# Kernel tuning notes

Measured on AMD Instinct MI355X. Metric: run time of the kernel, lower is better.

The kernel has to match this reference:

```python
import jax, jax.numpy as jnp
import numpy as np

N, B, E, H, G, L = 128, 2, 512, 1024, 50, 3
RBF_RADIUS = 12.0
AVG_LEN = 60.0


def _resmlp(h, Win, bin_, Wh, bh, Wout, bout):
    # input proj + activation, residual hidden blocks, linear head
    h = jax.nn.gelu(h @ Win + bin_, approximate=False)
    for i in range(Wh.shape[0]):  # fixed small number of layers
        h = h + jax.nn.gelu(h @ Wh[i] + bh[i], approximate=False)
    return h @ Wout + bout


def setup_inputs() -> dict:
    key = jax.random.key(0)
    ks = jax.random.split(key, 20)
    s_in = 1.0 / np.sqrt(3 * E)
    s_h = 1.0 / np.sqrt(H)
    s_g = 1.0 / np.sqrt(G)
    return {
        'x': jax.random.normal(ks[0], (N, B, E), jnp.float32),
        'dist': jax.random.uniform(ks[1], (N, N, B), jnp.float32),
        'vec_hat': jax.random.normal(ks[2], (N, N, B, 3), jnp.float32),
        'mask': jnp.ones((B, N), dtype=bool),
        'rbf_W': jax.random.normal(ks[3], (G, E), jnp.float32) * s_g,
        'rbf_b': jnp.zeros((E,), jnp.float32),
        'e_Win': jax.random.normal(ks[4], (3 * E, H), jnp.float32) * s_in,
        'e_bin': jnp.zeros((H,), jnp.float32),
        'e_Wh': jax.random.normal(ks[5], (L, H, H), jnp.float32) * s_h,
        'e_bh': jnp.zeros((L, H), jnp.float32),
        'e_Wout': jax.random.normal(ks[6], (H, 1), jnp.float32) * s_h,
        'e_bout': jnp.zeros((1,), jnp.float32),
        'f_Win': jax.random.normal(ks[7], (3 * E, H), jnp.float32) * s_in,
        'f_bin': jnp.zeros((H,), jnp.float32),
        'f_Wh': jax.random.normal(ks[8], (L, H, H), jnp.float32) * s_h,
        'f_bh': jnp.zeros((L, H), jnp.float32),
        'f_Wout': jax.random.normal(ks[9], (H, 1), jnp.float32) * s_h,
        'f_bout': jnp.zeros((1,), jnp.float32),
    }


def reference(x, dist, vec_hat, mask, rbf_W, rbf_b, e_Win, e_bin, e_Wh, e_bh,
              e_Wout, e_bout, f_Win, f_bin, f_Wh, f_bh, f_Wout, f_bout):
    # Gaussian RBF expansion + linear projection to embed_dim
    offset = jnp.linspace(0.0, RBF_RADIUS, G)
    coeff = -0.5 / (offset[1] - offset[0]) ** 2
    g = jnp.exp(coeff * (dist[..., None] - offset) ** 2)       # (N,N,B,G)
    rbf = g @ rbf_W + rbf_b                                    # (N,N,B,E)

    # all-pairs concat feature: [x_i, x_j, rbf_ij]  -> (N,N,B,3E)
    feat = jnp.concatenate([
        jnp.broadcast_to(x[:, None], rbf.shape),
        jnp.broadcast_to(x[None, :], rbf.shape),
        rbf,
    ], axis=-1)

    entries = (mask.T[:, None] & mask.T[None, :])[..., None].astype(feat.dtype)  # (N,N,B,1)

    energy_pairs = _resmlp(feat, e_Win, e_bin, e_Wh, e_bh, e_Wout, e_bout)       # (N,N,B,1)
    force_pairs = _resmlp(feat, f_Win, f_bin, f_Wh, f_bh, f_Wout, f_bout) * vec_hat  # (N,N,B,3)

    energy = (energy_pairs * entries).sum((0, 1)) / AVG_LEN ** 2  # (B,1)
    forces = (force_pairs * entries).sum(0) / AVG_LEN             # (N,B,3)
    # torch: forces.transpose(0,1)[mask]; mask is all-True here, so this is a reshape
    forces = jnp.swapaxes(forces, 0, 1).reshape(-1, 3)            # (B*N,3)
    return energy, forces
```

## Files before the change

### kernel.cpp

```cpp
#include <hip/hip_runtime.h>
#include <stdint.h>

typedef __bf16 bf16x8 __attribute__((ext_vector_type(8)));
typedef __bf16 bf16x4 __attribute__((ext_vector_type(4)));
typedef float  f32x4  __attribute__((ext_vector_type(4)));
typedef unsigned int u32;

__device__ __forceinline__ void gl_lds16(const void* gptr, void* lptr) {
    __builtin_amdgcn_global_load_lds(
        (const __attribute__((address_space(1))) u32*)gptr,
        (__attribute__((address_space(3))) u32*)lptr,
        16, 0, 0);
}

__device__ __forceinline__ float gelu_f(float x) {
    float u = 0.7978845608f * x * (1.0f + 0.044715f * x * x);
    float e = __expf(2.0f * u);
    float t = 1.0f - 2.0f / (e + 1.0f);
    return 0.5f * x * (1.0f + t);
}

#define MEMFENCE __asm__ __volatile__("" ::: "memory")

__global__ void zero_out(float* __restrict__ o, int n) {
    int i = blockIdx.x * 256 + threadIdx.x;
    if (i < n) o[i] = 0.0f;
}

__global__ __launch_bounds__(256)
void transpose_multi(const float* __restrict__ src0, const float* __restrict__ src1,
                     __bf16* __restrict__ dst0, __bf16* __restrict__ dst1,
                     int K, int Ncols, int perBranch) {
    const int z = blockIdx.z;
    const int branch = z / perBranch;
    const int l = z - branch * perBranch;
    const size_t elems = (size_t)K * Ncols;
    const float* src = (branch ? src1 : src0) + (size_t)l * elems;
    __bf16* dst = (branch ? dst1 : dst0) + (size_t)l * elems;

    __shared__ float tile[64][65];
    const int bk = blockIdx.x * 64;
    const int bn = blockIdx.y * 64;
    const int tid = threadIdx.x;
    const int tr = tid >> 4;
    const int tc = (tid & 15) * 4;
#pragma unroll
    for (int p = 0; p < 4; ++p) {
        const int r = tr + p * 16;
        float4 v = *(const float4*)&src[(size_t)(bk + r) * Ncols + bn + tc];
        tile[r][tc] = v.x; tile[r][tc + 1] = v.y;
        tile[r][tc + 2] = v.z; tile[r][tc + 3] = v.w;
    }
    __syncthreads();
#pragma unroll
    for (int p = 0; p < 4; ++p) {
        const int rn = tr + p * 16;
        bf16x4 o;
        o[0] = (__bf16)tile[tc + 0][rn];
        o[1] = (__bf16)tile[tc + 1][rn];
        o[2] = (__bf16)tile[tc + 2][rn];
        o[3] = (__bf16)tile[tc + 3][rn];
        *(bf16x4*)&dst[(size_t)(bn + rn) * K + bk + tc] = o;
    }
}

__global__ void f32_to_bf16(const float* __restrict__ s, __bf16* __restrict__ d, int n) {
    int idx = blockIdx.x * 256 + threadIdx.x;
    if (idx * 4 < n) {
        float4 v = *(const float4*)(s + idx * 4);
        bf16x4 o;
        o[0] = (__bf16)v.x; o[1] = (__bf16)v.y; o[2] = (__bf16)v.z; o[3] = (__bf16)v.w;
        *(bf16x4*)(d + idx * 4) = o;
    }
}

__global__ void build_M1(const float* __restrict__ rbfW, const float* __restrict__ rbf_b,
                         __bf16* __restrict__ M1) {
    int t = blockIdx.x * 256 + threadIdx.x;
    int r = t >> 8;
    int c = (t & 255) * 2;
    float v0 = 0.f, v1 = 0.f;
    if (r < 50)       { v0 = rbfW[r * 512 + c]; v1 = rbfW[r * 512 + c + 1]; }
    else if (r == 50) { v0 = rbf_b[c];          v1 = rbf_b[c + 1]; }
    M1[r * 512 + c] = (__bf16)v0;
    M1[r * 512 + c + 1] = (__bf16)v1;
}

__global__ __launch_bounds__(256)
void build_G(const float* __restrict__ dist, __bf16* __restrict__ G) {
    const int t = threadIdx.x;
    const int row = blockIdx.x * 32 + (t >> 3);
    const int c0 = (t & 7) * 8;
    const float sp = 12.0f / 49.0f;
    const float coeff = -0.5f / (sp * sp);
    const float d = dist[row];
    bf16x8 v;
#pragma unroll
    for (int q = 0; q < 8; ++q) {
        const int k = c0 + q;
        float val;
        if (k < 50)       { float tt = d - (float)k * sp; val = __expf(coeff * tt * tt); }
        else if (k == 50) val = 1.0f;
        else              val = 0.0f;
        v[q] = (__bf16)val;
    }
    *(bf16x8*)(G + (size_t)row * 64 + c0) = v;
}

template <int NK, int NBN, int MODE, bool DUAL, int MINW, bool SWZ>
__global__ __launch_bounds__(256, MINW)
void gemm_k(const __bf16* __restrict__ A0, const __bf16* __restrict__ A1,
            const __bf16* __restrict__ B0, const __bf16* __restrict__ B1,
            int lda, int ldb, int ldc,
            const float* __restrict__ bias0, const float* __restrict__ bias1,
            __bf16* __restrict__ C0, __bf16* __restrict__ C1,
            float* __restrict__ Cf0, float* __restrict__ Cf1,
            const float* __restrict__ P0, const float* __restrict__ P1,
            const float* __restrict__ wout0, const float* __restrict__ wout1,
            float* __restrict__ dot0, float* __restrict__ dot1) {
    constexpr int NBS = (NBN == 16) ? 4 : (NBN == 8) ? 3 : 0;
    __shared__ __align__(16) __bf16 As[3][128 * 32];
    __shared__ __align__(16) __bf16 Bs[3][128 * 32];

    const int tid = threadIdx.x;
    int bn, bm, branch = 0;
    if constexpr (SWZ) {
        const int x = blockIdx.x & 7;
        const int slot = blockIdx.x >> 3;
        bn = slot & (NBN - 1);
        int grp = x + ((slot >> NBS) << 3);
        if constexpr (DUAL) {
            const int half = (gridDim.x >> NBS) >> 1;
            branch = (grp >= half);
            if (branch) grp -= half;
        }
        bm = grp;
    } else {
        int f2 = blockIdx.x;
        if constexpr (DUAL) {
            const int half = gridDim.x >> 1;
            branch = (f2 >= half);
            if (branch) f2 -= half;
        }
        bn = f2 & (NBN - 1);
        bm = f2 >> NBS;
    }
    const int w = tid >> 6;
    const int lane = tid & 63;

    const __bf16* Ab = (DUAL && branch) ? A1 : A0;
    const __bf16* Bb = (DUAL && branch) ? B1 : B0;

    const int r0 = tid >> 2;
    const int s0 = tid & 3;
    const char* gA0 = (const char*)Ab + (size_t)(bm * 128 + r0) * lda + s0 * 16;
    const char* gA1 = gA0 + (size_t)64 * lda;
    const char* gB0 = (const char*)Bb + (size_t)(bn * 128 + r0) * ldb + s0 * 16;
    const char* gB1 = gB0 + (size_t)64 * ldb;

    char* lA0 = (char*)&As[0][0] + w * 1024;
    char* lA1 = (char*)&As[1][0] + w * 1024;
    char* lA2 = (char*)&As[2][0] + w * 1024;
    char* lB0 = (char*)&Bs[0][0] + w * 1024;
    char* lB1 = (char*)&Bs[1][0] + w * 1024;
    char* lB2 = (char*)&Bs[2][0] + w * 1024;

    const int wm = (w >> 1) & 1;
    const int wn = w & 1;
    const int lm = lane & 15;
    const int ko = (lane >> 4) << 3;
    const int fo = (wm * 64 + lm) * 32 + ko;
    const int go = (wn * 64 + lm) * 32 + ko;
    const __bf16* pA0 = &As[0][0] + fo;
    const __bf16* pA1 = &As[1][0] + fo;
    const __bf16* pA2 = &As[2][0] + fo;
    const __bf16* pB0 = &Bs[0][0] + go;
    const __bf16* pB1 = &Bs[1][0] + go;
    const __bf16* pB2 = &Bs[2][0] + go;

    f32x4 acc[4][4];
    const f32x4 zero = {0.0f, 0.0f, 0.0f, 0.0f};
#pragma unroll
    for (int i = 0; i < 4; ++i)
#pragma unroll
        for (int j = 0; j < 4; ++j) acc[i][j] = zero;

    auto stage = [&](int buf) {
        char* la = (buf == 0) ? lA0 : (buf == 1) ? lA1 : lA2;
        char* lb = (buf == 0) ? lB0 : (buf == 1) ? lB1 : lB2;
        gl_lds16(gA0, la); gl_lds16(gA1, la + 4096);
        gl_lds16(gB0, lb); gl_lds16(gB1, lb + 4096);
        gA0 += 64; gA1 += 64; gB0 += 64; gB1 += 64;
    };
    auto compute = [&](int buf) {
        const __bf16* pa = (buf == 0) ? pA0 : (buf == 1) ? pA1 : pA2;
        const __bf16* pb = (buf == 0) ? pB0 : (buf == 1) ? pB1 : pB2;
        bf16x8 af[4], bfg[4];
#pragma unroll
        for (int i = 0; i < 4; ++i) {
            af[i]  = *(const bf16x8*)(pa + i * 512);
            bfg[i] = *(const bf16x8*)(pb + i * 512);
        }
#pragma unroll
        for (int mi = 0; mi < 4; ++mi)
#pragma unroll
            for (int ni = 0; ni < 4; ++ni)
                acc[mi][ni] = __builtin_amdgcn_mfma_f32_16x16x32_bf16(
                    af[mi], bfg[ni], acc[mi][ni], 0, 0, 0);
    };
    auto iterstep = [&](int cbuf, int sbuf) {
        MEMFENCE;
        __builtin_amdgcn_s_waitcnt(0xF74);
        __builtin_amdgcn_s_barrier();
        MEMFENCE;
        compute(cbuf);
        MEMFENCE;
        stage(sbuf);
        MEMFENCE;
    };

    stage(0);
    stage(1);
    constexpr int NIT = NK - 2;
    constexpr int NG = NIT / 3;
    constexpr int NR = NIT % 3;
    for (int g = 0; g < NG; ++g) {
        iterstep(0, 2);
        iterstep(1, 0);
        iterstep(2, 1);
    }
    if constexpr (NR >= 1) iterstep(0, 2);
    if constexpr (NR >= 2) iterstep(1, 0);
    MEMFENCE;
    __builtin_amdgcn_s_waitcnt(0xF74);
    __builtin_amdgcn_s_barrier();
    MEMFENCE;
    compute((NK - 2) % 3);
    MEMFENCE;
    __builtin_amdgcn_s_waitcnt(0xF70);
    __builtin_amdgcn_s_barrier();
    MEMFENCE;
    compute((NK - 1) % 3);

    const int col0 = bn * 128 + wn * 64 + lm;
    const int row0 = bm * 128 + wm * 64 + ((lane >> 4) << 2);
    const int ldaE = lda >> 1;

    float rowdot[16];
    if constexpr (MODE == 1) {
#pragma unroll
        for (int q = 0; q < 16; ++q) rowdot[q] = 0.0f;
    }

    const bool side = (MODE == 2) && (bn >= 8);
    const float* bp = (MODE == 2) ? (side ? bias1 : bias0)
                                  : ((DUAL && branch) ? bias1 : bias0);
    __bf16* Cout = (MODE == 2) ? (side ? C1 : C0)
                               : ((DUAL && branch) ? C1 : C0);
    const float* woutb = (MODE == 1) ? ((DUAL && branch) ? wout1 : wout0) : nullptr;

#pragma unroll
    for (int ni = 0; ni < 4; ++ni) {
        const int gn = col0 + ni * 16;
        const int gnl = (MODE == 2) ? (gn & 1023) : gn;
        float bv = 0.0f;
        if constexpr (MODE <= 2) bv = bp[gnl];
        float wv = 0.0f;
        if constexpr (MODE == 1) wv = woutb[gn];

        float res[16];
        if constexpr (MODE == 0 || MODE == 1) {
#pragma unroll
            for (int mi = 0; mi < 4; ++mi)
#pragma unroll
                for (int rr = 0; rr < 4; ++rr)
                    res[mi * 4 + rr] =
                        (float)Ab[(size_t)(row0 + mi * 16 + rr) * ldaE + gn];
        } else if constexpr (MODE == 2) {
#pragma unroll
            for (int mi = 0; mi < 4; ++mi)
#pragma unroll
                for (int rr = 0; rr < 4; ++rr) {
                    const int gm = row0 + mi * 16 + rr;
                    const int p0row = ((gm >> 8) << 1) | (gm & 1);
                    const int p1row = gm & 255;
                    res[mi * 4 + rr] = P0[(size_t)p0row * 2048 + gn]
                                     + P1[(size_t)p1row * 2048 + gn];
                }
        }
        MEMFENCE;

#pragma unroll
        for (int mi = 0; mi < 4; ++mi) {
#pragma unroll
            for (int rr = 0; rr < 4; ++rr) {
                const int gm = row0 + mi * 16 + rr;
                const float a = acc[mi][ni][rr];
                if constexpr (MODE == 0) {
                    float v = gelu_f(a + bv) + res[mi * 4 + rr];
                    Cout[(size_t)gm * ldc + gn] = (__bf16)v;
                } else if constexpr (MODE == 1) {
                    float v = gelu_f(a + bv) + res[mi * 4 + rr];
                    rowdot[mi * 4 + rr] += v * wv;
                } else if constexpr (MODE == 2) {
                    float v = a + bv + res[mi * 4 + rr];
                    Cout[(size_t)gm * ldc + gnl] = (__bf16)gelu_f(v);
                } else if constexpr (MODE == 3) {
                    float* Cfw = (DUAL && branch) ? Cf1 : Cf0;
                    Cfw[(size_t)gm * ldc + gn] = a;
                } else {
                    C0[(size_t)gm * ldc + gn] = (__bf16)a;
                }
            }
        }
    }

    if constexpr (MODE == 1) {
#pragma unroll
        for (int s = 1; s < 16; s <<= 1)
#pragma unroll
            for (int q = 0; q < 16; ++q) rowdot[q] += __shfl_xor(rowdot[q], s);
        if (lm == 0) {
            float* dotb = (DUAL && branch) ? dot1 : dot0;
            float* dp = dotb + (size_t)(bn * 2 + wn) * 32768 + row0;
#pragma unroll
            for (int q = 0; q < 16; ++q)
                dp[(q >> 2) * 16 + (q & 3)] = rowdot[q];
        }
    }
}

#define WBAR(imm) do { MEMFENCE; __builtin_amdgcn_s_waitcnt(imm); \
                       __builtin_amdgcn_s_barrier(); MEMFENCE; } while (0)

template <int MODE, bool DUAL>
__global__ __launch_bounds__(512, 2)
void gemm256(const __bf16* __restrict__ A0, const __bf16* __restrict__ A1,
             const __bf16* __restrict__ B0, const __bf16* __restrict__ B1,
             const float* __restrict__ bias0, const float* __restrict__ bias1,
             __bf16* __restrict__ C0, __bf16* __restrict__ C1,
             const float* __restrict__ wout0, const float* __restrict__ wout1,
             float* __restrict__ dot0, float* __restrict__ dot1) {
    __shared__ __align__(16) char ldsbuf[131072];

    const int tid = threadIdx.x;
    const int nxg = gridDim.x >> 3;
    const int id = (blockIdx.x & 7) * nxg + (blockIdx.x >> 3);
    const int bn = id & 3;
    int rest = id >> 2;
    int branch = 0;
    if constexpr (DUAL) { branch = rest >> 7; rest &= 127; }
    const int bm = rest;

    const __bf16* __restrict__ Ab = (DUAL && branch) ? A1 : A0;
    const __bf16* __restrict__ Bb = (DUAL && branch) ? B1 : B0;

    const int w = tid >> 6;
    const int lane = tid & 63;

    const int srow = tid >> 2;
    const int scol = ((tid & 3) << 4) ^ (((tid >> 3) & 3) << 4);
    const char* gA = (const char*)Ab + (size_t)(bm * 256 + srow) * 2048 + scol;
    const char* gB = (const char*)Bb + (size_t)(bn * 256 + srow) * 2048 + scol;

    auto stageA = [&](int kt, int buf) {
        const size_t ko = (size_t)kt * 64;
        char* d = ldsbuf + buf * 32768 + w * 1024;
        gl_lds16(gA + ko,          d);
        gl_lds16(gA + ko + 262144, d + 8192);
    };
    auto stageB = [&](int kt, int buf) {
        const size_t ko = (size_t)kt * 64;
        char* d = ldsbuf + buf * 32768 + w * 1024;
        gl_lds16(gB + ko,          d + 16384);
        gl_lds16(gB + ko + 262144, d + 24576);
    };

    const int wm = w >> 2, wn = w & 3;
    const int lm = lane & 15, lq = lane >> 4;
    const int swz = ((lm >> 1) & 3) << 4;
    const int rA = (wm * 128 + lm) * 64 + ((lq * 16) ^ swz);
    const int rB = 16384 + (wn * 64 + lm) * 64 + ((lq * 16) ^ swz);

    f32x4 acc[8][4];
    const f32x4 zero = {0.0f, 0.0f, 0.0f, 0.0f};
#pragma unroll
    for (int i = 0; i < 8; ++i)
#pragma unroll
        for (int j = 0; j < 4; ++j) acc[i][j] = zero;

    auto body = [&](int kt, int cbuf, int sbuf, bool dostage) {
        const char* Lb = ldsbuf + cbuf * 32768;
        MEMFENCE;
        bf16x8 a[8], b[4];
#pragma unroll
        for (int ni = 0; ni < 4; ++ni)
            b[ni] = *(const bf16x8*)(Lb + rB + ni * 1024);
#pragma unroll
        for (int mi = 0; mi < 4; ++mi)
            a[mi] = *(const bf16x8*)(Lb + rA + mi * 1024);
        if (dostage) stageA(kt + 3, sbuf);
        MEMFENCE;
        __builtin_amdgcn_s_waitcnt(0xC07F);
        MEMFENCE;
        __builtin_amdgcn_s_setprio(1);
#pragma unroll
        for (int mi = 0; mi < 4; ++mi)
#pragma unroll
            for (int ni = 0; ni < 4; ++ni)
                acc[mi][ni] = __builtin_amdgcn_mfma_f32_16x16x32_bf16(
                    a[mi], b[ni], acc[mi][ni], 0, 0, 0);
        __builtin_amdgcn_s_setprio(0);
        __builtin_amdgcn_s_barrier();
        MEMFENCE;
#pragma unroll
        for (int mi = 4; mi < 8; ++mi)
            a[mi] = *(const bf16x8*)(Lb + rA + mi * 1024);
        if (dostage) stageB(kt + 3, sbuf);
        MEMFENCE;
        __builtin_amdgcn_s_waitcnt(0xC07F);
        MEMFENCE;
        __builtin_amdgcn_s_setprio(1);
#pragma unroll
        for (int mi = 4; mi < 8; ++mi)
#pragma unroll
            for (int ni = 0; ni < 4; ++ni)
                acc[mi][ni] = __builtin_amdgcn_mfma_f32_16x16x32_bf16(
                    a[mi], b[ni], acc[mi][ni], 0, 0, 0);
        __builtin_amdgcn_s_setprio(0);
    };

    stageA(0, 0); stageB(0, 0);
    stageA(1, 1); stageB(1, 1);
    stageA(2, 2); stageB(2, 2);

    for (int g = 0; g < 7; ++g) {
        const int k0 = g * 4;
        WBAR(0xF78); body(k0 + 0, 0, 3, true);
        WBAR(0xF78); body(k0 + 1, 1, 0, true);
        WBAR(0xF78); body(k0 + 2, 2, 1, true);
        WBAR(0xF78); body(k0 + 3, 3, 2, true);
    }
    WBAR(0xF78); body(28, 0, 3, true);
    WBAR(0xF78); body(29, 1, 0, false);
    WBAR(0xF74); body(30, 2, 1, false);
    WBAR(0xF70); body(31, 3, 2, false);

    const int row0 = bm * 256 + wm * 128 + lq * 4;
    const int col0 = bn * 256 + wn * 64 + lm;
    const float* __restrict__ bp = (DUAL && branch) ? bias1 : bias0;
    float bv[4];
#pragma unroll
    for (int ni = 0; ni < 4; ++ni) bv[ni] = bp[col0 + ni * 16];

    if constexpr (MODE == 0) {
        __bf16* __restrict__ Cw = (DUAL && branch) ? C1 : C0;
#pragma unroll
        for (int mi = 0; mi < 8; ++mi) {
            float res[16];
#pragma unroll
            for (int ni = 0; ni < 4; ++ni)
#pragma unroll
                for (int rr = 0; rr < 4; ++rr)
                    res[ni * 4 + rr] =
                        (float)Ab[(size_t)(row0 + mi * 16 + rr) * 1024 + col0 + ni * 16];
            MEMFENCE;
#pragma unroll
            for (int ni = 0; ni < 4; ++ni)
#pragma unroll
                for (int rr = 0; rr < 4; ++rr) {
                    float v = gelu_f(acc[mi][ni][rr] + bv[ni]) + res[ni * 4 + rr];
                    Cw[(size_t)(row0 + mi * 16 + rr) * 1024 + col0 + ni * 16] = (__bf16)v;
                }
        }
    } else {
        const float* __restrict__ wb = (DUAL && branch) ? wout1 : wout0;
        float wv[4];
#pragma unroll
        for (int ni = 0; ni < 4; ++ni) wv[ni] = wb[col0 + ni * 16];
        float rowdot[32];
#pragma unroll
        for (int q = 0; q < 32; ++q) rowdot[q] = 0.0f;
#pragma unroll
        for (int mi = 0; mi < 8; ++mi) {
            float res[16];
#pragma unroll
            for (int ni = 0; ni < 4; ++ni)
#pragma unroll
                for (int rr = 0; rr < 4; ++rr)
                    res[ni * 4 + rr] =
                        (float)Ab[(size_t)(row0 + mi * 16 + rr) * 1024 + col0 + ni * 16];
            MEMFENCE;
#pragma unroll
            for (int ni = 0; ni < 4; ++ni)
#pragma unroll
                for (int rr = 0; rr < 4; ++rr) {
                    float v = gelu_f(acc[mi][ni][rr] + bv[ni]) + res[ni * 4 + rr];
                    rowdot[mi * 4 + rr] += v * wv[ni];
                }
        }
#pragma unroll
        for (int s = 1; s < 16; s <<= 1)
#pragma unroll
            for (int q = 0; q < 32; ++q) rowdot[q] += __shfl_xor(rowdot[q], s);
        if (lm == 0) {
            float* __restrict__ db = (DUAL && branch) ? dot1 : dot0;
            float* dp = db + (size_t)(bn * 4 + wn) * 32768 + bm * 256 + wm * 128;
#pragma unroll
            for (int mi = 0; mi < 8; ++mi)
#pragma unroll
                for (int rr = 0; rr < 4; ++rr)
                    dp[mi * 16 + lq * 4 + rr] = rowdot[mi * 4 + rr];
        }
    }
}

__global__ __launch_bounds__(128)
void finalize(const float* __restrict__ dot_e, const float* __restrict__ dot_f,
              const float* __restrict__ eb, const float* __restrict__ fb,
              const float* __restrict__ vec, float* __restrict__ out) {
    const int bj = blockIdx.x;
    const int bb = bj >> 7, jj = bj & 127;
    const int i = threadIdx.x;
    const int m = (i * 128 + jj) * 2 + bb;
    float e = eb[0], f = fb[0];
#pragma unroll
    for (int s = 0; s < 16; ++s) {
        e += dot_e[(size_t)s * 32768 + m];
        f += dot_f[(size_t)s * 32768 + m];
    }
    f *= (1.0f / 60.0f);
    float fx = f * vec[(size_t)m * 3 + 0];
    float fy = f * vec[(size_t)m * 3 + 1];
    float fz = f * vec[(size_t)m * 3 + 2];
#pragma unroll
    for (int off = 32; off > 0; off >>= 1) {
        e  += __shfl_down(e, off);
        fx += __shfl_down(fx, off);
        fy += __shfl_down(fy, off);
        fz += __shfl_down(fz, off);
    }
    __shared__ float red[2][4];
    const int wv = i >> 6, lane = i & 63;
    if (lane == 0) { red[wv][0] = e; red[wv][1] = fx; red[wv][2] = fy; red[wv][3] = fz; }
    __syncthreads();
    if (i == 0) {
        atomicAdd(&out[bb], (red[0][0] + red[1][0]) * (1.0f / 3600.0f));
        float* fo = out + 2 + bj * 3;
        fo[0] = red[0][1] + red[1][1];
        fo[1] = red[0][2] + red[1][2];
        fo[2] = red[0][3] + red[1][3];
    }
}

extern "C" void kernel_launch(void* const* d_in, const int* in_sizes, int n_in,
                              void* d_out, int out_size, void* d_ws, size_t ws_size,
                              hipStream_t stream) {
    const float* x     = (const float*)d_in[0];
    const float* dist  = (const float*)d_in[1];
    const float* vec   = (const float*)d_in[2];
    const float* rbfW  = (const float*)d_in[4];
    const float* rbf_b = (const float*)d_in[5];
    const float* eWin  = (const float*)d_in[6];
    const float* ebin  = (const float*)d_in[7];
    const float* eWh   = (const float*)d_in[8];
    const float* ebh   = (const float*)d_in[9];
    const float* eWout = (const float*)d_in[10];
    const float* ebout = (const float*)d_in[11];
    const float* fWin  = (const float*)d_in[12];
    const float* fbin  = (const float*)d_in[13];
    const float* fWh   = (const float*)d_in[14];
    const float* fbh   = (const float*)d_in[15];
    const float* fWout = (const float*)d_in[16];
    const float* fbout = (const float*)d_in[17];
    float* out = (float*)d_out;

    char* p = (char*)d_ws;
    __bf16* WinTcat = (__bf16*)p;
    __bf16* eWinT = WinTcat;          p += (size_t)1024 * 1536 * 2;
    __bf16* fWinT = (__bf16*)p;       p += (size_t)1024 * 1536 * 2;
    __bf16* eWhT0 = (__bf16*)p;       p += (size_t)3 * 1024 * 1024 * 2;
    __bf16* fWhT0 = (__bf16*)p;       p += (size_t)3 * 1024 * 1024 * 2;
    __bf16* xb  = (__bf16*)p;         p += (size_t)256 * 512 * 2;
    __bf16* M1  = (__bf16*)p;         p += (size_t)128 * 512 * 2;
    __bf16* WgT = (__bf16*)p;         p += (size_t)2048 * 128 * 2;
    __bf16* G   = (__bf16*)p;         p += (size_t)32768 * 64 * 2;
    float* P0   = (float*)p;          p += (size_t)256 * 2048 * 4;
    float* P1   = (float*)p;          p += (size_t)256 * 2048 * 4;
    float* dot_e = (float*)p;         p += (size_t)16 * 32768 * 4;
    float* dot_f = (float*)p;         p += (size_t)16 * 32768 * 4;
    const size_t SLAB = (size_t)32768 * 1024 * 2;
    __bf16* he0 = (__bf16*)p;         p += SLAB;
    __bf16* hf0 = (__bf16*)p;         p += SLAB;
    __bf16* hAe = (__bf16*)p;         p += SLAB;
    __bf16* hAf = hAe;
    const bool dualHidden = ((size_t)(p - (char*)d_ws) + SLAB) <= ws_size;
    if (dualHidden) hAf = (__bf16*)p;

    zero_out<<<dim3(4), dim3(256), 0, stream>>>(out, 770);

    transpose_multi<<<dim3(24, 16, 2), dim3(256), 0, stream>>>(
        eWin, fWin, eWinT, fWinT, 1536, 1024, 1);
    transpose_multi<<<dim3(16, 16, 6), dim3(256), 0, stream>>>(
        eWh, fWh, eWhT0, fWhT0, 1024, 1024, 3);
    f32_to_bf16<<<dim3(128), dim3(256), 0, stream>>>(x, xb, 131072);
    build_M1<<<dim3(128), dim3(256), 0, stream>>>(rbfW, rbf_b, M1);
    build_G<<<dim3(1024), dim3(256), 0, stream>>>(dist, G);

    const dim3 blk(256);
    gemm_k<16, 16, 3, true, 3, false><<<dim3(64), blk, 0, stream>>>(
        xb, xb, WinTcat, WinTcat + 512, 1024, 3072, 2048,
        nullptr, nullptr, nullptr, nullptr, P0, P1,
        nullptr, nullptr, nullptr, nullptr, nullptr, nullptr);
    gemm_k<16, 1, 4, false, 3, false><<<dim3(16), blk, 0, stream>>>(
        WinTcat + 1024, nullptr, M1, nullptr, 3072, 1024, 128,
        nullptr, nullptr, WgT, nullptr, nullptr, nullptr,
        nullptr, nullptr, nullptr, nullptr, nullptr, nullptr);
    gemm_k<2, 16, 2, false, 3, true><<<dim3(4096), blk, 0, stream>>>(
        G, nullptr, WgT, nullptr, 128, 256, 1024,
        ebin, fbin, he0, hf0, nullptr, nullptr, P0, P1,
        nullptr, nullptr, nullptr, nullptr);

    const dim3 blk512(512);
    if (dualHidden) {
        gemm256<0, true><<<dim3(1024), blk512, 0, stream>>>(
            he0, hf0, eWhT0, fWhT0, ebh + 0, fbh + 0,
            hAe, hAf, nullptr, nullptr, nullptr, nullptr);
        gemm256<0, true><<<dim3(1024), blk512, 0, stream>>>(
            hAe, hAf, eWhT0 + (size_t)1048576, fWhT0 + (size_t)1048576,
            ebh + 1024, fbh + 1024, he0, hf0, nullptr, nullptr, nullptr, nullptr);
        gemm256<1, true><<<dim3(1024), blk512, 0, stream>>>(
            he0, hf0, eWhT0 + (size_t)2 * 1048576, fWhT0 + (size_t)2 * 1048576,
            ebh + 2048, fbh + 2048, nullptr, nullptr,
            eWout, fWout, dot_e, dot_f);
    } else {
        gemm256<0, false><<<dim3(512), blk512, 0, stream>>>(
            he0, nullptr, eWhT0, nullptr, ebh + 0, nullptr,
            hAe, nullptr, nullptr, nullptr, nullptr, nullptr);
        gemm256<0, false><<<dim3(512), blk512, 0, stream>>>(
            hAe, nullptr, eWhT0 + (size_t)1048576, nullptr, ebh + 1024, nullptr,
            he0, nullptr, nullptr, nullptr, nullptr, nullptr);
        gemm256<1, false><<<dim3(512), blk512, 0, stream>>>(
            he0, nullptr, eWhT0 + (size_t)2 * 1048576, nullptr, ebh + 2048, nullptr,
            nullptr, nullptr, eWout, nullptr, dot_e, nullptr);
        gemm256<0, false><<<dim3(512), blk512, 0, stream>>>(
            hf0, nullptr, fWhT0, nullptr, fbh + 0, nullptr,
            hAf, nullptr, nullptr, nullptr, nullptr, nullptr);
        gemm256<0, false><<<dim3(512), blk512, 0, stream>>>(
            hAf, nullptr, fWhT0 + (size_t)1048576, nullptr, fbh + 1024, nullptr,
            hf0, nullptr, nullptr, nullptr, nullptr, nullptr);
        gemm256<1, false><<<dim3(512), blk512, 0, stream>>>(
            hf0, nullptr, fWhT0 + (size_t)2 * 1048576, nullptr, fbh + 2048, nullptr,
            nullptr, nullptr, fWout, nullptr, dot_f, nullptr);
    }

    finalize<<<dim3(256), dim3(128), 0, stream>>>(dot_e, dot_f, ebout, fbout, vec, out);
}
```

Baseline: 737.4 us.

## Route RBF input-projection GEMM through the 256x256 MFMA tile kernel with fused epilogue

Generalizes gemm256 with template parameters for N-block count, K-tile count and leading dimensions, and adds a MODE 2 epilogue that adds bias plus the precomputed x_i/x_j projections (P0, P1), applies GELU and writes both energy and force hidden states. The small-K (K=128) input projection previously ran on the generic gemm_k kernel with 4096 small blocks. It now uses the LDS-staged 256x256 MFMA kernel with only two K tiles. The short K loop leaves little room for pipelining, and the epilogue does scattered P1 loads.

```diff
diff --git a/kernel.cpp b/kernel.cpp
--- a/kernel.cpp
+++ b/kernel.cpp
@@ -333,21 +333,24 @@
 #define WBAR(imm) do { MEMFENCE; __builtin_amdgcn_s_waitcnt(imm); \
                        __builtin_amdgcn_s_barrier(); MEMFENCE; } while (0)
 
-template <int MODE, bool DUAL>
+template <int MODE, bool DUAL, int NBN, int NT, int LDA, int LDB>
 __global__ __launch_bounds__(512, 2)
 void gemm256(const __bf16* __restrict__ A0, const __bf16* __restrict__ A1,
              const __bf16* __restrict__ B0, const __bf16* __restrict__ B1,
              const float* __restrict__ bias0, const float* __restrict__ bias1,
              __bf16* __restrict__ C0, __bf16* __restrict__ C1,
              const float* __restrict__ wout0, const float* __restrict__ wout1,
-             float* __restrict__ dot0, float* __restrict__ dot1) {
-    __shared__ __align__(16) char ldsbuf[131072];
+             float* __restrict__ dot0, float* __restrict__ dot1,
+             const float* __restrict__ P0, const float* __restrict__ P1) {
+    constexpr int NBUF = (NT >= 3) ? 4 : 2;
+    constexpr int NBS = (NBN == 8) ? 3 : 2;
+    __shared__ __align__(16) char ldsbuf[NBUF * 32768];
 
     const int tid = threadIdx.x;
     const int nxg = gridDim.x >> 3;
     const int id = (blockIdx.x & 7) * nxg + (blockIdx.x >> 3);
-    const int bn = id & 3;
-    int rest = id >> 2;
+    const int bn = id & (NBN - 1);
+    int rest = id >> NBS;
     int branch = 0;
     if constexpr (DUAL) { branch = rest >> 7; rest &= 127; }
     const int bm = rest;
@@ -360,20 +363,20 @@
 
     const int srow = tid >> 2;
     const int scol = ((tid & 3) << 4) ^ (((tid >> 3) & 3) << 4);
-    const char* gA = (const char*)Ab + (size_t)(bm * 256 + srow) * 2048 + scol;
-    const char* gB = (const char*)Bb + (size_t)(bn * 256 + srow) * 2048 + scol;
+    const char* gA = (const char*)Ab + (size_t)(bm * 256 + srow) * LDA + scol;
+    const char* gB = (const char*)Bb + (size_t)(bn * 256 + srow) * LDB + scol;
 
     auto stageA = [&](int kt, int buf) {
         const size_t ko = (size_t)kt * 64;
         char* d = ldsbuf + buf * 32768 + w * 1024;
-        gl_lds16(gA + ko,          d);
-        gl_lds16(gA + ko + 262144, d + 8192);
+        gl_lds16(gA + ko,             d);
+        gl_lds16(gA + ko + 128 * LDA, d + 8192);
     };
     auto stageB = [&](int kt, int buf) {
         const size_t ko = (size_t)kt * 64;
         char* d = ldsbuf + buf * 32768 + w * 1024;
-        gl_lds16(gB + ko,          d + 16384);
-        gl_lds16(gB + ko + 262144, d + 24576);
+        gl_lds16(gB + ko,             d + 16384);
+        gl_lds16(gB + ko + 128 * LDB, d + 24576);
     };
 
     const int wm = w >> 2, wn = w & 3;
@@ -430,24 +433,68 @@
         __builtin_amdgcn_s_setprio(0);
     };
 
-    stageA(0, 0); stageB(0, 0);
-    stageA(1, 1); stageB(1, 1);
-    stageA(2, 2); stageB(2, 2);
-
-    for (int g = 0; g < 7; ++g) {
-        const int k0 = g * 4;
-        WBAR(0xF78); body(k0 + 0, 0, 3, true);
-        WBAR(0xF78); body(k0 + 1, 1, 0, true);
-        WBAR(0xF78); body(k0 + 2, 2, 1, true);
-        WBAR(0xF78); body(k0 + 3, 3, 2, true);
-    }
-    WBAR(0xF78); body(28, 0, 3, true);
-    WBAR(0xF78); body(29, 1, 0, false);
-    WBAR(0xF74); body(30, 2, 1, false);
-    WBAR(0xF70); body(31, 3, 2, false);
+    if constexpr (NT == 32) {
+        stageA(0, 0); stageB(0, 0);
+        stageA(1, 1); stageB(1, 1);
+        stageA(2, 2); stageB(2, 2);
+        for (int g = 0; g < 7; ++g) {
+            const int k0 = g * 4;
+            WBAR(0xF78); body(k0 + 0, 0, 3, true);
+            WBAR(0xF78); body(k0 + 1, 1, 0, true);
+            WBAR(0xF78); body(k0 + 2, 2, 1, true);
+            WBAR(0xF78); body(k0 + 3, 3, 2, true);
+        }
+        WBAR(0xF78); body(28, 0, 3, true);
+        WBAR(0xF78); body(29, 1, 0, false);
+        WBAR(0xF74); body(30, 2, 1, false);
+        WBAR(0xF70); body(31, 3, 2, false);
+    } else {
+        stageA(0, 0); stageB(0, 0);
+        stageA(1, 1); stageB(1, 1);
+        WBAR(0xF74); body(0, 0, 0, false);
+        WBAR(0xF70); body(1, 1, 0, false);
+    }
 
     const int row0 = bm * 256 + wm * 128 + lq * 4;
     const int col0 = bn * 256 + wn * 64 + lm;
+
+    if constexpr (MODE == 2) {
+        const bool side = (bn >= (NBN >> 1));
+        const float* __restrict__ bp = side ? bias1 : bias0;
+        __bf16* __restrict__ Cw = side ? C1 : C0;
+        float bv[4], p0v[2][4];
+#pragma unroll
+        for (int ni = 0; ni < 4; ++ni) {
+            const int gn = col0 + ni * 16;
+            bv[ni] = bp[gn & 1023];
+            p0v[0][ni] = P0[(size_t)(bm << 1) * 2048 + gn];
+            p0v[1][ni] = P0[(size_t)((bm << 1) | 1) * 2048 + gn];
+        }
+#pragma unroll
+        for (int mi = 0; mi < 8; ++mi) {
+            float p1v[16];
+#pragma unroll
+            for (int rr = 0; rr < 4; ++rr) {
+                const int p1row = (wm * 128 + lq * 4 + mi * 16 + rr) & 255;
+#pragma unroll
+                for (int ni = 0; ni < 4; ++ni)
+                    p1v[rr * 4 + ni] = P1[(size_t)p1row * 2048 + col0 + ni * 16];
+            }
+            MEMFENCE;
+#pragma unroll
+            for (int ni = 0; ni < 4; ++ni)
+#pragma unroll
+                for (int rr = 0; rr < 4; ++rr) {
+                    const int gm = row0 + mi * 16 + rr;
+                    float v = acc[mi][ni][rr] + bv[ni] + p0v[rr & 1][ni]
+                            + p1v[rr * 4 + ni];
+                    Cw[(size_t)gm * 1024 + ((col0 + ni * 16) & 1023)] =
+                        (__bf16)gelu_f(v);
+                }
+        }
+        return;
+    }
+
     const float* __restrict__ bp = (DUAL && branch) ? bias1 : bias0;
     float bv[4];
 #pragma unroll
@@ -473,7 +520,7 @@
                     Cw[(size_t)(row0 + mi * 16 + rr) * 1024 + col0 + ni * 16] = (__bf16)v;
                 }
         }
-    } else {
+    } else if constexpr (MODE == 1) {
         const float* __restrict__ wb = (DUAL && branch) ? wout1 : wout0;
         float wv[4];
 #pragma unroll
@@ -616,42 +663,43 @@
         WinTcat + 1024, nullptr, M1, nullptr, 3072, 1024, 128,
         nullptr, nullptr, WgT, nullptr, nullptr, nullptr,
         nullptr, nullptr, nullptr, nullptr, nullptr, nullptr);
-    gemm_k<2, 16, 2, false, 3, true><<<dim3(4096), blk, 0, stream>>>(
-        G, nullptr, WgT, nullptr, 128, 256, 1024,
-        ebin, fbin, he0, hf0, nullptr, nullptr, P0, P1,
-        nullptr, nullptr, nullptr, nullptr);
 
     const dim3 blk512(512);
+    gemm256<2, false, 8, 2, 128, 256><<<dim3(1024), blk512, 0, stream>>>(
+        G, nullptr, WgT, nullptr, ebin, fbin, he0, hf0,
+        nullptr, nullptr, nullptr, nullptr, P0, P1);
+
     if (dualHidden) {
-        gemm256<0, true><<<dim3(1024), blk512, 0, stream>>>(
+        gemm256<0, true, 4, 32, 2048, 2048><<<dim3(1024), blk512, 0, stream>>>(
             he0, hf0, eWhT0, fWhT0, ebh + 0, fbh + 0,
-            hAe, hAf, nullptr, nullptr, nullptr, nullptr);
-        gemm256<0, true><<<dim3(1024), blk512, 0, stream>>>(
+            hAe, hAf, nullptr, nullptr, nullptr, nullptr, nullptr, nullptr);
+        gemm256<0, true, 4, 32, 2048, 2048><<<dim3(1024), blk512, 0, stream>>>(
             hAe, hAf, eWhT0 + (size_t)1048576, fWhT0 + (size_t)1048576,
-            ebh + 1024, fbh + 1024, he0, hf0, nullptr, nullptr, nullptr, nullptr);
-        gemm256<1, true><<<dim3(1024), blk512, 0, stream>>>(
+            ebh + 1024, fbh + 1024, he0, hf0,
+            nullptr, nullptr, nullptr, nullptr, nullptr, nullptr);
+        gemm256<1, true, 4, 32, 2048, 2048><<<dim3(1024), blk512, 0, stream>>>(
             he0, hf0, eWhT0 + (size_t)2 * 1048576, fWhT0 + (size_t)2 * 1048576,
             ebh + 2048, fbh + 2048, nullptr, nullptr,
-            eWout, fWout, dot_e, dot_f);
+            eWout, fWout, dot_e, dot_f, nullptr, nullptr);
     } else {
-        gemm256<0, false><<<dim3(512), blk512, 0, stream>>>(
+        gemm256<0, false, 4, 32, 2048, 2048><<<dim3(512), blk512, 0, stream>>>(
             he0, nullptr, eWhT0, nullptr, ebh + 0, nullptr,
-            hAe, nullptr, nullptr, nullptr, nullptr, nullptr);
-        gemm256<0, false><<<dim3(512), blk512, 0, stream>>>(
+            hAe, nullptr, nullptr, nullptr, nullptr, nullptr, nullptr, nullptr);
+        gemm256<0, false, 4, 32, 2048, 2048><<<dim3(512), blk512, 0, stream>>>(
             hAe, nullptr, eWhT0 + (size_t)1048576, nullptr, ebh + 1024, nullptr,
-            he0, nullptr, nullptr, nullptr, nullptr, nullptr);
-        gemm256<1, false><<<dim3(512), blk512, 0, stream>>>(
+            he0, nullptr, nullptr, nullptr, nullptr, nullptr, nullptr, nullptr);
+        gemm256<1, false, 4, 32, 2048, 2048><<<dim3(512), blk512, 0, stream>>>(
             he0, nullptr, eWhT0 + (size_t)2 * 1048576, nullptr, ebh + 2048, nullptr,
-            nullptr, nullptr, eWout, nullptr, dot_e, nullptr);
-        gemm256<0, false><<<dim3(512), blk512, 0, stream>>>(
+            nullptr, nullptr, eWout, nullptr, dot_e, nullptr, nullptr, nullptr);
+        gemm256<0, false, 4, 32, 2048, 2048><<<dim3(512), blk512, 0, stream>>>(
             hf0, nullptr, fWhT0, nullptr, fbh + 0, nullptr,
-            hAf, nullptr, nullptr, nullptr, nullptr, nullptr);
-        gemm256<0, false><<<dim3(512), blk512, 0, stream>>>(
+            hAf, nullptr, nullptr, nullptr, nullptr, nullptr, nullptr, nullptr);
+        gemm256<0, false, 4, 32, 2048, 2048><<<dim3(512), blk512, 0, stream>>>(
             hAf, nullptr, fWhT0 + (size_t)1048576, nullptr, fbh + 1024, nullptr,
-            hf0, nullptr, nullptr, nullptr, nullptr, nullptr);
-        gemm256<1, false><<<dim3(512), blk512, 0, stream>>>(
+            hf0, nullptr, nullptr, nullptr, nullptr, nullptr, nullptr, nullptr);
+        gemm256<1, false, 4, 32, 2048, 2048><<<dim3(512), blk512, 0, stream>>>(
             hf0, nullptr, fWhT0 + (size_t)2 * 1048576, nullptr, fbh + 2048, nullptr,
-            nullptr, nullptr, fWout, nullptr, dot_f, nullptr);
+            nullptr, nullptr, fWout, nullptr, dot_f, nullptr, nullptr, nullptr);
     }
 
     finalize<<<dim3(256), dim3(128), 0, stream>>>(dot_e, dot_f, ebout, fbout, vec, out);
```

Result: slower. 761.1 us (+3.2%).
